# Optimization experiments

Measured on AMD Instinct MI355X. Metric: run time of the kernel, lower is better.

The kernel has to match this reference:

```python
import jax, jax.numpy as jnp
import numpy as np

NEG_BIG = -1.0e9


def setup_inputs() -> dict:
    key = jax.random.key(0)
    kq, kk, kv, km = jax.random.split(key, 4)
    B, Lq, Lk, D = 16, 2048, 2048, 128
    queries = jax.random.normal(kq, (B, Lq, D), dtype=jnp.float32)
    keys = jax.random.normal(kk, (B, Lk, D), dtype=jnp.float32)
    values = jax.random.normal(kv, (B, Lk, D), dtype=jnp.float32)
    mask = (jax.random.uniform(km, (Lk,)) > 0.8).astype(jnp.float32)
    return {"queries": queries, "keys": keys, "values": values, "mask": mask}


def reference(queries, keys, values, mask):
    d = keys.shape[-1]
    # scores: [B, Lq, Lk]
    scores = jnp.einsum("bqd,bkd->bqk", queries, keys) / jnp.sqrt(jnp.float32(d))
    masked = scores + mask[None, None, :] * NEG_BIG
    attn = jax.nn.softmax(masked, axis=-1)
    # dropout is identity in eval / p=0.0
    return jnp.einsum("bqk,bkd->bqd", attn, values)
```

## Files before the change

kernel.cpp:

```cpp
#include <hip/hip_runtime.h>
#include <hip/hip_bf16.h>


#define B_    16
#define LQ_   2048
#define LK_   2048
#define DIM_  128
#define NTH   256
#define SCALE_ 0.08838834764831845f
#define LOG2E_ 1.4426950408889634f
#define SC2_   (SCALE_ * LOG2E_)
#define NEGBIG -1.0e9f
#define PS 72

typedef __attribute__((ext_vector_type(8))) short bf16x8;
typedef __attribute__((ext_vector_type(4))) float f32x4;

#define GLDS(gsrc, ldst) \
  __builtin_amdgcn_global_load_lds( \
      (const __attribute__((address_space(1))) unsigned int*)(gsrc), \
      (__attribute__((address_space(3))) unsigned int*)(ldst), 16, 0, 0)

static __device__ __forceinline__ unsigned short f2bf(float f) {
    unsigned int u = __builtin_bit_cast(unsigned int, f);
    u += 0x7fff + ((u >> 16) & 1);
    return (unsigned short)(u >> 16);
}

__global__ __launch_bounds__(256) void build_idx(const float* __restrict__ Mk,
                                                 int* __restrict__ hdr,
                                                 int* __restrict__ idx)
{
    __shared__ int sc[256];
    int t = threadIdx.x;
    int keep[8], loc[8];
    int c = 0;
    #pragma unroll
    for (int j = 0; j < 8; ++j) {
        keep[j] = (Mk[t * 8 + j] < 0.5f) ? 1 : 0;
        loc[j] = c;
        c += keep[j];
    }
    sc[t] = c;
    __syncthreads();
    for (int off = 1; off < 256; off <<= 1) {
        int v = (t >= off) ? sc[t - off] : 0;
        __syncthreads();
        sc[t] += v;
        __syncthreads();
    }
    int base = sc[t] - c;
    #pragma unroll
    for (int j = 0; j < 8; ++j)
        if (keep[j]) idx[base + loc[j]] = t * 8 + j;
    if (t == 255) hdr[0] = sc[255];
}

__global__ __launch_bounds__(NTH) void pack_kv(
    const float* __restrict__ K, const float* __restrict__ V,
    const int* __restrict__ hdr, const int* __restrict__ idx,
    unsigned short* __restrict__ Kb, unsigned short* __restrict__ Vtb)
{
    const int cnt = hdr[0];
    int bid = blockIdx.x;
    if (bid < 2048) {
        int gid = bid * NTH + threadIdx.x;
        int c  = gid & 15;
        int r2 = (gid >> 4) & 63;
        int T  = gid >> 10;
        int slot = (r2 & 32) + 2 * (r2 & 15) + ((r2 >> 4) & 1);
        int j = (T & 31) * 64 + slot;
        int key = (j < cnt) ? idx[j] : 0;
        const float4* s4 = (const float4*)(K + ((size_t)(T >> 5) * LK_ + key) * DIM_ + c * 8);
        float4 a = s4[0], bq = s4[1];
        bf16x8 h = { (short)f2bf(a.x),  (short)f2bf(a.y),  (short)f2bf(a.z),  (short)f2bf(a.w),
                     (short)f2bf(bq.x), (short)f2bf(bq.y), (short)f2bf(bq.z), (short)f2bf(bq.w) };
        *(bf16x8*)(Kb + (size_t)T * 8192 + r2 * 128 + ((c ^ (r2 & 15)) * 8)) = h;
    } else {
        int T = bid - 2048;
        int w4 = threadIdx.x >> 6, lane = threadIdx.x & 63;
        const float* vb = V + (size_t)(T >> 5) * LK_ * DIM_;
        const int* ix = idx + (T & 31) * 64;
        int jbase = (T & 31) * 64;
        unsigned short* db = Vtb + (size_t)T * 8192;
        #pragma unroll
        for (int half = 0; half < 2; ++half) {
            int d = half * 64 + lane;
            #pragma unroll
            for (int cb = 0; cb < 8; cb += 4) {
                int c = cb + w4;
                float v[8];
                #pragma unroll
                for (int kk = 0; kk < 8; ++kk) {
                    int j = c * 8 + kk;
                    int key = (jbase + j < cnt) ? ix[j] : 0;
                    v[kk] = vb[(size_t)key * DIM_ + d];
                }
                bf16x8 h = { (short)f2bf(v[0]), (short)f2bf(v[1]), (short)f2bf(v[2]), (short)f2bf(v[3]),
                             (short)f2bf(v[4]), (short)f2bf(v[5]), (short)f2bf(v[6]), (short)f2bf(v[7]) };
                *(bf16x8*)(db + (c >> 2) * 4096 + d * 32 + (c & 3) * 8) = h;
            }
        }
    }
}

__global__ __launch_bounds__(NTH, 2) void attn_mfma6(
    const float* __restrict__ Q, const unsigned short* __restrict__ Kb,
    const unsigned short* __restrict__ Vtb, const int* __restrict__ hdr,
    float* __restrict__ O)
{
    __shared__ __align__(16) unsigned short sKa[8192];
    __shared__ __align__(16) unsigned short sKb_[8192];
    __shared__ __align__(16) unsigned short sP[64 * PS];
    __shared__ float sLp[64];

    const int tid  = threadIdx.x;
    const int w    = tid >> 6, lane = tid & 63;
    const int quad = lane >> 4, l15 = lane & 15;
    const int rg   = (w & 1) * 32;
    const int wh   = w >> 1;
    const int kh   = wh * 32;

    const int bid = blockIdx.x;
    const int grp = bid >> 3;
    const int b   = (bid & 7) + 8 * (grp & 1);
    const int q0  = (grp >> 1) * 64;

    const int cnt = hdr[0];
    const int nIter2 = (((cnt + 63) >> 6) + 1) & ~1;

    bf16x8 vone;
    #pragma unroll
    for (int j = 0; j < 8; ++j) vone[j] = (short)0x3F80;

    const int voff = wh * 4096 + l15 * 32 + quad * 8;

    bf16x8 aQ[2][4];
    {
        const float4* Qg = (const float4*)(Q + ((size_t)b * LQ_ + q0) * DIM_);
        #pragma unroll
        for (int h = 0; h < 2; ++h) {
            #pragma unroll
            for (int it = 0; it < 4; ++it) {
                int i2 = tid + it * NTH;
                int r = i2 >> 5, c4 = i2 & 31;
                float4 v = Qg[(h * 32 + r) * 32 + c4];
                ushort4 hh = { f2bf(v.x * SC2_), f2bf(v.y * SC2_),
                               f2bf(v.z * SC2_), f2bf(v.w * SC2_) };
                *(ushort4*)&sP[r * 128 + (((c4 >> 1) ^ (r & 15)) * 8) + (c4 & 1) * 4] = hh;
            }
            __syncthreads();
            if ((rg >> 5) == h) {
                #pragma unroll
                for (int rs = 0; rs < 2; ++rs)
                    #pragma unroll
                    for (int ks = 0; ks < 4; ++ks)
                        aQ[rs][ks] = *(const bf16x8*)&sP[(rs * 16 + l15) * 128 +
                                                         (((ks * 4 + quad) ^ l15) * 8)];
            }
            __syncthreads();
        }
    }

    {
        const char* ksrc = (const char*)Kb + (size_t)(b * 32) * 16384;
        #pragma unroll
        for (int j = 0; j < 4; ++j) {
            int o = (j * 4 + w) * 1024;
            GLDS(ksrc + o + lane * 16, (char*)sKa + o);
        }
    }
    __syncthreads();

    f32x4 acc[2][8], lacc[2];
    #pragma unroll
    for (int rs = 0; rs < 2; ++rs) {
        lacc[rs] = (f32x4){0.f, 0.f, 0.f, 0.f};
        #pragma unroll
        for (int dt = 0; dt < 8; ++dt) acc[rs][dt] = (f32x4){0.f, 0.f, 0.f, 0.f};
    }

#define TILE_BODY(CURK, NXTK, I) do {                                          \
         \
    const unsigned short* vsrc = Vtb + (size_t)(b * 32 + (I)) * 8192 + voff;   \
    bf16x8 bv[8];                                                              \
    _Pragma("unroll")                                                          \
    for (int dt = 0; dt < 8; ++dt) bv[dt] = *(const bf16x8*)(vsrc + dt * 512); \
    const int nxt = (I) + 1;                                                   \
    if (nxt < nIter2) {                                                        \
        const char* ksrc = (const char*)Kb + (size_t)(b * 32 + nxt) * 16384;   \
        _Pragma("unroll")                                                      \
        for (int j = 0; j < 4; ++j) {                                          \
            int o = (j * 4 + w) * 1024;                                        \
            GLDS(ksrc + o + lane * 16, (char*)(NXTK) + o);                     \
        }                                                                      \
    }                                                                          \
    f32x4 s_[2][2];                                                            \
    _Pragma("unroll")                                                          \
    for (int kt2 = 0; kt2 < 2; ++kt2) {                                        \
        f32x4 c0 = (f32x4){0.f,0.f,0.f,0.f}, c1 = (f32x4){0.f,0.f,0.f,0.f};   \
        _Pragma("unroll")                                                      \
        for (int ks = 0; ks < 4; ++ks) {                                       \
            bf16x8 bk = *(const bf16x8*)&(CURK)[(kh + kt2 * 16 + l15) * 128 +  \
                                                (((ks * 4 + quad) ^ l15) * 8)];\
            c0 = __builtin_amdgcn_mfma_f32_16x16x32_bf16(aQ[0][ks], bk, c0, 0,0,0); \
            c1 = __builtin_amdgcn_mfma_f32_16x16x32_bf16(aQ[1][ks], bk, c1, 0,0,0); \
        }                                                                      \
        int slot = (I) * 64 + kh + 2 * l15 + kt2;                              \
        bool kept = slot < cnt;                                                \
        _Pragma("unroll")                                                      \
        for (int r = 0; r < 4; ++r) {                                          \
            s_[0][kt2][r] = kept ? c0[r] : -1.0e30f;                           \
            s_[1][kt2][r] = kept ? c1[r] : -1.0e30f;                           \
        }                                                                      \
    }                                                                          \
    _Pragma("unroll")                                                          \
    for (int rs = 0; rs < 2; ++rs)                                             \
        _Pragma("unroll")                                                      \
        for (int r = 0; r < 4; ++r) {                                          \
            float p0 = __builtin_amdgcn_exp2f(s_[rs][0][r]);                   \
            float p1 = __builtin_amdgcn_exp2f(s_[rs][1][r]);                   \
            int row = rg + rs * 16 + quad * 4 + r;                             \
            unsigned pk = __builtin_amdgcn_perm(                               \
                __builtin_bit_cast(unsigned, p1),                              \
                __builtin_bit_cast(unsigned, p0), 0x07060302u);                \
            *(unsigned*)&sP[row * PS + kh + 2 * l15] = pk;                     \
        }                                                                      \
    {                                                                          \
        bf16x8 aP0 = *(const bf16x8*)&sP[(rg + l15) * PS + kh + quad * 8];     \
        bf16x8 aP1 = *(const bf16x8*)&sP[(rg + 16 + l15) * PS + kh + quad * 8];\
        lacc[0] = __builtin_amdgcn_mfma_f32_16x16x32_bf16(aP0, vone, lacc[0], 0,0,0); \
        lacc[1] = __builtin_amdgcn_mfma_f32_16x16x32_bf16(aP1, vone, lacc[1], 0,0,0); \
        _Pragma("unroll")                                                      \
        for (int dt = 0; dt < 8; ++dt) {                                       \
            acc[0][dt] = __builtin_amdgcn_mfma_f32_16x16x32_bf16(aP0, bv[dt], acc[0][dt], 0,0,0); \
            acc[1][dt] = __builtin_amdgcn_mfma_f32_16x16x32_bf16(aP1, bv[dt], acc[1][dt], 0,0,0); \
        }                                                                      \
    }                                                                          \
    __syncthreads();                                                           \
} while (0)

    for (int kk = 0; kk < nIter2; kk += 2) {
        TILE_BODY(sKa,  sKb_, kk);
        TILE_BODY(sKb_, sKa,  kk + 1);
    }
#undef TILE_BODY

    float* sOw = (rg == 0) ? (float*)sKa : (float*)sKb_;
    if (wh == 1) {
        #pragma unroll
        for (int rs = 0; rs < 2; ++rs)
            #pragma unroll
            for (int r = 0; r < 4; ++r) {
                int lrow = rs * 16 + quad * 4 + r;
                #pragma unroll
                for (int dt = 0; dt < 8; ++dt)
                    sOw[lrow * 128 + dt * 16 + l15] = acc[rs][dt][r];
                if (l15 == 0) sLp[rg + lrow] = lacc[rs][r];
            }
    }
    __syncthreads();
    if (wh == 0) {
        float* Og = O + ((size_t)b * LQ_ + q0 + rg) * DIM_;
        #pragma unroll
        for (int rs = 0; rs < 2; ++rs)
            #pragma unroll
            for (int r = 0; r < 4; ++r) {
                int lrow = rs * 16 + quad * 4 + r;
                float inv = 1.0f / (lacc[rs][r] + sLp[rg + lrow]);
                #pragma unroll
                for (int dt = 0; dt < 8; ++dt)
                    Og[(size_t)lrow * DIM_ + dt * 16 + l15] =
                        (acc[rs][dt][r] + sOw[lrow * 128 + dt * 16 + l15]) * inv;
            }
    }
}

#define QS 136
#define VS 72
__global__ __launch_bounds__(NTH, 2) void attn_fallback(
    const float* __restrict__ Q, const float* __restrict__ K,
    const float* __restrict__ V, const float* __restrict__ Mk,
    float* __restrict__ O)
{
    __shared__ __align__(16) unsigned short sQ[64][QS];
    __shared__ __align__(16) unsigned short sK[64][QS];
    __shared__ __align__(16) unsigned short sVt[DIM_][VS];
    __shared__ __align__(16) unsigned short sPf[64][VS];
    __shared__ float sB[64];

    const int tid  = threadIdx.x;
    const int w    = tid >> 6, lane = tid & 63;
    const int quad = lane >> 4, l15 = lane & 15;
    const int bid = blockIdx.x;
    const int grp = bid >> 3;
    const int b   = (bid & 7) + 8 * (grp & 1);
    const int q0  = (grp >> 1) * 64;

    {
        const float4* Qg = (const float4*)(Q + ((size_t)b * LQ_ + q0) * DIM_);
        #pragma unroll
        for (int it = 0; it < 8; ++it) {
            int i = tid + it * NTH;
            int r = i >> 5, c4 = i & 31;
            float4 v = Qg[r * 32 + c4];
            ushort4 h = { f2bf(v.x), f2bf(v.y), f2bf(v.z), f2bf(v.w) };
            *(ushort4*)&sQ[r][c4 * 4] = h;
        }
    }
    __syncthreads();
    bf16x8 aQ[4];
    #pragma unroll
    for (int ks = 0; ks < 4; ++ks)
        aQ[ks] = *(const bf16x8*)&sQ[w * 16 + l15][ks * 32 + quad * 8];

    float m_i[4], l_i[4];
    f32x4 acc[8];
    #pragma unroll
    for (int r = 0; r < 4; ++r) { m_i[r] = -3.0e38f; l_i[r] = 0.f; }
    #pragma unroll
    for (int dt = 0; dt < 8; ++dt) acc[dt] = (f32x4){0.f, 0.f, 0.f, 0.f};

    for (int k0 = 0; k0 < LK_; k0 += 64) {
        const float4* Kg = (const float4*)(K + ((size_t)b * LK_ + k0) * DIM_);
        const float4* Vg = (const float4*)(V + ((size_t)b * LK_ + k0) * DIM_);
        #pragma unroll
        for (int it = 0; it < 8; ++it) {
            int i = tid + it * NTH;
            int r = i >> 5, c4 = i & 31;
            float4 kv = Kg[r * 32 + c4];
            ushort4 h = { f2bf(kv.x), f2bf(kv.y), f2bf(kv.z), f2bf(kv.w) };
            *(ushort4*)&sK[r][c4 * 4] = h;
            float4 vv = Vg[r * 32 + c4];
            int d = c4 * 4;
            sVt[d + 0][r] = f2bf(vv.x);
            sVt[d + 1][r] = f2bf(vv.y);
            sVt[d + 2][r] = f2bf(vv.z);
            sVt[d + 3][r] = f2bf(vv.w);
        }
        if (tid < 64) sB[tid] = Mk[k0 + tid] * NEGBIG;
        __syncthreads();

        f32x4 s[4];
        #pragma unroll
        for (int kt = 0; kt < 4; ++kt) {
            f32x4 c = (f32x4){0.f, 0.f, 0.f, 0.f};
            #pragma unroll
            for (int ks = 0; ks < 4; ++ks) {
                bf16x8 bk = *(const bf16x8*)&sK[kt * 16 + l15][ks * 32 + quad * 8];
                c = __builtin_amdgcn_mfma_f32_16x16x32_bf16(aQ[ks], bk, c, 0, 0, 0);
            }
            float bias = sB[kt * 16 + l15];
            #pragma unroll
            for (int r = 0; r < 4; ++r) s[kt][r] = c[r] * SCALE_ + bias;
        }
        #pragma unroll
        for (int r = 0; r < 4; ++r) {
            float mx = fmaxf(fmaxf(s[0][r], s[1][r]), fmaxf(s[2][r], s[3][r]));
            #pragma unroll
            for (int off = 1; off < 16; off <<= 1) mx = fmaxf(mx, __shfl_xor(mx, off));
            float mn = fmaxf(m_i[r], mx);
            float al = __expf(m_i[r] - mn);
            m_i[r] = mn;
            float rsum = 0.f;
            #pragma unroll
            for (int kt = 0; kt < 4; ++kt) {
                float p = __expf(s[kt][r] - mn);
                rsum += p;
                sPf[w * 16 + quad * 4 + r][kt * 16 + l15] = f2bf(p);
            }
            #pragma unroll
            for (int off = 1; off < 16; off <<= 1) rsum += __shfl_xor(rsum, off);
            l_i[r] = l_i[r] * al + rsum;
            #pragma unroll
            for (int dt = 0; dt < 8; ++dt) acc[dt][r] *= al;
        }
        bf16x8 aP0 = *(const bf16x8*)&sPf[w * 16 + l15][quad * 8];
        bf16x8 aP1 = *(const bf16x8*)&sPf[w * 16 + l15][32 + quad * 8];
        #pragma unroll
        for (int dt = 0; dt < 8; ++dt) {
            bf16x8 bv0 = *(const bf16x8*)&sVt[dt * 16 + l15][quad * 8];
            bf16x8 bv1 = *(const bf16x8*)&sVt[dt * 16 + l15][32 + quad * 8];
            acc[dt] = __builtin_amdgcn_mfma_f32_16x16x32_bf16(aP0, bv0, acc[dt], 0, 0, 0);
            acc[dt] = __builtin_amdgcn_mfma_f32_16x16x32_bf16(aP1, bv1, acc[dt], 0, 0, 0);
        }
        __syncthreads();
    }
    float* Og = O + ((size_t)b * LQ_ + q0 + w * 16) * DIM_;
    #pragma unroll
    for (int r = 0; r < 4; ++r) {
        float inv = 1.0f / l_i[r];
        int row = quad * 4 + r;
        #pragma unroll
        for (int dt = 0; dt < 8; ++dt)
            Og[(size_t)row * DIM_ + dt * 16 + l15] = acc[dt][r] * inv;
    }
}

extern "C" void kernel_launch(void* const* d_in, const int* in_sizes, int n_in,
                              void* d_out, int out_size, void* d_ws, size_t ws_size,
                              hipStream_t stream)
{
    const float* Q  = (const float*)d_in[0];
    const float* K  = (const float*)d_in[1];
    const float* V  = (const float*)d_in[2];
    const float* Mk = (const float*)d_in[3];
    float* O = (float*)d_out;

    const size_t seg  = (size_t)B_ * LK_ * DIM_ * 2;
    const size_t need = 16384 + 2 * seg;
    if (ws_size >= need) {
        int* hdr = (int*)d_ws;
        int* idx = hdr + 16;
        unsigned short* Kb  = (unsigned short*)((char*)d_ws + 16384);
        unsigned short* Vtb = Kb + seg / 2;
        hipLaunchKernelGGL(build_idx, dim3(1),    dim3(256), 0, stream, Mk, hdr, idx);
        hipLaunchKernelGGL(pack_kv,   dim3(2560), dim3(NTH), 0, stream, K, V, hdr, idx, Kb, Vtb);
        hipLaunchKernelGGL(attn_mfma6, dim3(512), dim3(NTH), 0, stream, Q, Kb, Vtb, hdr, O);
    } else {
        hipLaunchKernelGGL(attn_fallback, dim3(512), dim3(NTH), 0, stream, Q, K, V, Mk, O);
    }
}
```

Baseline: 144.5 us.

## Fuse mask compaction into packing and stream K fragments directly to registers

Merges the single-block index build and the K/V packing kernel into one kernel. Each block recomputes the mask prefix scan in shared memory and transposes V through LDS. K is now stored in MFMA-fragment order, so the attention kernel loads K and V straight into double-buffered registers instead of staging K through LDS with global_load_lds. This removes one launch and the per-tile block barriers. The cost is more registers (risking occupancy at launch bounds 2) and redundant scans across 512 blocks.

New measurement: 155.4 us. 7.5% more time.

```diff
diff --git a/kernel.cpp b/kernel.cpp
--- a/kernel.cpp
+++ b/kernel.cpp
@@ -16,102 +16,96 @@
 typedef __attribute__((ext_vector_type(8))) short bf16x8;
 typedef __attribute__((ext_vector_type(4))) float f32x4;
 
-#define GLDS(gsrc, ldst) \
-  __builtin_amdgcn_global_load_lds( \
-      (const __attribute__((address_space(1))) unsigned int*)(gsrc), \
-      (__attribute__((address_space(3))) unsigned int*)(ldst), 16, 0, 0)
-
 static __device__ __forceinline__ unsigned short f2bf(float f) {
     unsigned int u = __builtin_bit_cast(unsigned int, f);
     u += 0x7fff + ((u >> 16) & 1);
     return (unsigned short)(u >> 16);
 }
 
-__global__ __launch_bounds__(256) void build_idx(const float* __restrict__ Mk,
-                                                 int* __restrict__ hdr,
-                                                 int* __restrict__ idx)
+__global__ __launch_bounds__(NTH) void pack_all(
+    const float* __restrict__ K, const float* __restrict__ V,
+    const float* __restrict__ Mk, int* __restrict__ hdr,
+    unsigned short* __restrict__ Kb, unsigned short* __restrict__ Vtb)
 {
+    __shared__ int sIdx[2048];
     __shared__ int sc[256];
-    int t = threadIdx.x;
+    __shared__ unsigned short sV[64 * 136];
+
+    const int tid = threadIdx.x;
+    const int T = blockIdx.x;
+    const int b = T >> 5, t = T & 31;
+
     int keep[8], loc[8];
     int c = 0;
     #pragma unroll
     for (int j = 0; j < 8; ++j) {
-        keep[j] = (Mk[t * 8 + j] < 0.5f) ? 1 : 0;
+        keep[j] = (Mk[tid * 8 + j] < 0.5f) ? 1 : 0;
         loc[j] = c;
         c += keep[j];
     }
-    sc[t] = c;
+    sc[tid] = c;
     __syncthreads();
     for (int off = 1; off < 256; off <<= 1) {
-        int v = (t >= off) ? sc[t - off] : 0;
+        int v = (tid >= off) ? sc[tid - off] : 0;
         __syncthreads();
-        sc[t] += v;
+        sc[tid] += v;
         __syncthreads();
     }
-    int base = sc[t] - c;
+    const int base = sc[tid] - c;
     #pragma unroll
     for (int j = 0; j < 8; ++j)
-        if (keep[j]) idx[base + loc[j]] = t * 8 + j;
-    if (t == 255) hdr[0] = sc[255];
+        if (keep[j]) sIdx[base + loc[j]] = tid * 8 + j;
+    __syncthreads();
+    const int cnt = sc[255];
+    if (T == 0 && tid == 0) hdr[0] = cnt;
+
+    const float* Kbase = K + (size_t)b * LK_ * DIM_;
+    unsigned short* kdst = Kb + (size_t)T * 8192;
+    #pragma unroll
+    for (int it = 0; it < 8; ++it) {
+        int i = tid + it * NTH;
+        int sp = i >> 5, c4 = i & 31;
+        int wh = sp >> 5, kt2 = (sp >> 4) & 1, l15 = sp & 15;
+        int g = t * 64 + wh * 32 + 2 * l15 + kt2;
+        int key = (g < cnt) ? sIdx[g] : 0;
+        float4 v = *(const float4*)(Kbase + (size_t)key * DIM_ + c4 * 4);
+        ushort4 h = { f2bf(v.x), f2bf(v.y), f2bf(v.z), f2bf(v.w) };
+        int ks = c4 >> 3, quad = (c4 >> 1) & 3;
+        *(ushort4*)(kdst + wh * 4096 + kt2 * 2048 + ks * 512 +
+                    quad * 128 + l15 * 8 + (c4 & 1) * 4) = h;
+    }
+
+    const float* Vbase = V + (size_t)b * LK_ * DIM_;
+    #pragma unroll
+    for (int it = 0; it < 8; ++it) {
+        int i = tid + it * NTH;
+        int slot = i >> 5, c4 = i & 31;
+        int g = t * 64 + slot;
+        int key = (g < cnt) ? sIdx[g] : 0;
+        float4 v = *(const float4*)(Vbase + (size_t)key * DIM_ + c4 * 4);
+        ushort4 h = { f2bf(v.x), f2bf(v.y), f2bf(v.z), f2bf(v.w) };
+        *(ushort4*)&sV[slot * 136 + c4 * 4] = h;
+    }
+    __syncthreads();
+    unsigned short* vdst = Vtb + (size_t)T * 8192;
+    const int d = tid & 127, wh2 = tid >> 7;
+    #pragma unroll
+    for (int quad = 0; quad < 4; ++quad) {
+        bf16x8 h;
+        #pragma unroll
+        for (int j = 0; j < 8; ++j)
+            h[j] = (short)sV[(wh2 * 32 + quad * 8 + j) * 136 + d];
+        *(bf16x8*)(vdst + wh2 * 4096 + d * 32 + quad * 8) = h;
+    }
 }
 
-__global__ __launch_bounds__(NTH) void pack_kv(
-    const float* __restrict__ K, const float* __restrict__ V,
-    const int* __restrict__ hdr, const int* __restrict__ idx,
-    unsigned short* __restrict__ Kb, unsigned short* __restrict__ Vtb)
-{
-    const int cnt = hdr[0];
-    int bid = blockIdx.x;
-    if (bid < 2048) {
-        int gid = bid * NTH + threadIdx.x;
-        int c  = gid & 15;
-        int r2 = (gid >> 4) & 63;
-        int T  = gid >> 10;
-        int slot = (r2 & 32) + 2 * (r2 & 15) + ((r2 >> 4) & 1);
-        int j = (T & 31) * 64 + slot;
-        int key = (j < cnt) ? idx[j] : 0;
-        const float4* s4 = (const float4*)(K + ((size_t)(T >> 5) * LK_ + key) * DIM_ + c * 8);
-        float4 a = s4[0], bq = s4[1];
-        bf16x8 h = { (short)f2bf(a.x),  (short)f2bf(a.y),  (short)f2bf(a.z),  (short)f2bf(a.w),
-                     (short)f2bf(bq.x), (short)f2bf(bq.y), (short)f2bf(bq.z), (short)f2bf(bq.w) };
-        *(bf16x8*)(Kb + (size_t)T * 8192 + r2 * 128 + ((c ^ (r2 & 15)) * 8)) = h;
-    } else {
-        int T = bid - 2048;
-        int w4 = threadIdx.x >> 6, lane = threadIdx.x & 63;
-        const float* vb = V + (size_t)(T >> 5) * LK_ * DIM_;
-        const int* ix = idx + (T & 31) * 64;
-        int jbase = (T & 31) * 64;
-        unsigned short* db = Vtb + (size_t)T * 8192;
-        #pragma unroll
-        for (int half = 0; half < 2; ++half) {
-            int d = half * 64 + lane;
-            #pragma unroll
-            for (int cb = 0; cb < 8; cb += 4) {
-                int c = cb + w4;
-                float v[8];
-                #pragma unroll
-                for (int kk = 0; kk < 8; ++kk) {
-                    int j = c * 8 + kk;
-                    int key = (jbase + j < cnt) ? ix[j] : 0;
-                    v[kk] = vb[(size_t)key * DIM_ + d];
-                }
-                bf16x8 h = { (short)f2bf(v[0]), (short)f2bf(v[1]), (short)f2bf(v[2]), (short)f2bf(v[3]),
-                             (short)f2bf(v[4]), (short)f2bf(v[5]), (short)f2bf(v[6]), (short)f2bf(v[7]) };
-                *(bf16x8*)(db + (c >> 2) * 4096 + d * 32 + (c & 3) * 8) = h;
-            }
-        }
-    }
-}
-
-__global__ __launch_bounds__(NTH, 2) void attn_mfma6(
+__global__ __launch_bounds__(NTH, 2) void attn_mfma7(
     const float* __restrict__ Q, const unsigned short* __restrict__ Kb,
     const unsigned short* __restrict__ Vtb, const int* __restrict__ hdr,
     float* __restrict__ O)
 {
-    __shared__ __align__(16) unsigned short sKa[8192];
-    __shared__ __align__(16) unsigned short sKb_[8192];
     __shared__ __align__(16) unsigned short sP[64 * PS];
+    __shared__ float sO[64 * 128];
     __shared__ float sLp[64];
 
     const int tid  = threadIdx.x;
@@ -134,6 +128,7 @@
     for (int j = 0; j < 8; ++j) vone[j] = (short)0x3F80;
 
     const int voff = wh * 4096 + l15 * 32 + quad * 8;
+    const int koff = wh * 4096 + lane * 8;
 
     bf16x8 aQ[2][4];
     {
@@ -162,16 +157,6 @@
         }
     }
 
-    {
-        const char* ksrc = (const char*)Kb + (size_t)(b * 32) * 16384;
-        #pragma unroll
-        for (int j = 0; j < 4; ++j) {
-            int o = (j * 4 + w) * 1024;
-            GLDS(ksrc + o + lane * 16, (char*)sKa + o);
-        }
-    }
-    __syncthreads();
-
     f32x4 acc[2][8], lacc[2];
     #pragma unroll
     for (int rs = 0; rs < 2; ++rs) {
@@ -180,31 +165,30 @@
         for (int dt = 0; dt < 8; ++dt) acc[rs][dt] = (f32x4){0.f, 0.f, 0.f, 0.f};
     }
 
-#define TILE_BODY(CURK, NXTK, I) do {                                          \
-         \
-    const unsigned short* vsrc = Vtb + (size_t)(b * 32 + (I)) * 8192 + voff;   \
-    bf16x8 bv[8];                                                              \
+#define LOADKV(DK, DV, I) do {                                                 \
+    const unsigned short* kbp = Kb + (size_t)(b * 32 + (I)) * 8192 + koff;     \
     _Pragma("unroll")                                                          \
-    for (int dt = 0; dt < 8; ++dt) bv[dt] = *(const bf16x8*)(vsrc + dt * 512); \
+    for (int kt2 = 0; kt2 < 2; ++kt2)                                          \
+        _Pragma("unroll")                                                      \
+        for (int ks = 0; ks < 4; ++ks)                                         \
+            DK[kt2][ks] = *(const bf16x8*)(kbp + kt2 * 2048 + ks * 512);       \
+    const unsigned short* vbp = Vtb + (size_t)(b * 32 + (I)) * 8192 + voff;    \
+    _Pragma("unroll")                                                          \
+    for (int dt = 0; dt < 8; ++dt)                                             \
+        DV[dt] = *(const bf16x8*)(vbp + dt * 512);                             \
+} while (0)
+
+#define TILE_BODY(CK, CV, NK, NV, I) do {                                      \
     const int nxt = (I) + 1;                                                   \
-    if (nxt < nIter2) {                                                        \
-        const char* ksrc = (const char*)Kb + (size_t)(b * 32 + nxt) * 16384;   \
-        _Pragma("unroll")                                                      \
-        for (int j = 0; j < 4; ++j) {                                          \
-            int o = (j * 4 + w) * 1024;                                        \
-            GLDS(ksrc + o + lane * 16, (char*)(NXTK) + o);                     \
-        }                                                                      \
-    }                                                                          \
+    if (nxt < nIter2) LOADKV(NK, NV, nxt);                                     \
     f32x4 s_[2][2];                                                            \
     _Pragma("unroll")                                                          \
     for (int kt2 = 0; kt2 < 2; ++kt2) {                                        \
         f32x4 c0 = (f32x4){0.f,0.f,0.f,0.f}, c1 = (f32x4){0.f,0.f,0.f,0.f};   \
         _Pragma("unroll")                                                      \
         for (int ks = 0; ks < 4; ++ks) {                                       \
-            bf16x8 bk = *(const bf16x8*)&(CURK)[(kh + kt2 * 16 + l15) * 128 +  \
-                                                (((ks * 4 + quad) ^ l15) * 8)];\
-            c0 = __builtin_amdgcn_mfma_f32_16x16x32_bf16(aQ[0][ks], bk, c0, 0,0,0); \
-            c1 = __builtin_amdgcn_mfma_f32_16x16x32_bf16(aQ[1][ks], bk, c1, 0,0,0); \
+            c0 = __builtin_amdgcn_mfma_f32_16x16x32_bf16(aQ[0][ks], CK[kt2][ks], c0, 0,0,0); \
+            c1 = __builtin_amdgcn_mfma_f32_16x16x32_bf16(aQ[1][ks], CK[kt2][ks], c1, 0,0,0); \
         }                                                                      \
         int slot = (I) * 64 + kh + 2 * l15 + kt2;                              \
         bool kept = slot < cnt;                                                \
@@ -233,30 +217,31 @@
         lacc[1] = __builtin_amdgcn_mfma_f32_16x16x32_bf16(aP1, vone, lacc[1], 0,0,0); \
         _Pragma("unroll")                                                      \
         for (int dt = 0; dt < 8; ++dt) {                                       \
-            acc[0][dt] = __builtin_amdgcn_mfma_f32_16x16x32_bf16(aP0, bv[dt], acc[0][dt], 0,0,0); \
-            acc[1][dt] = __builtin_amdgcn_mfma_f32_16x16x32_bf16(aP1, bv[dt], acc[1][dt], 0,0,0); \
+            acc[0][dt] = __builtin_amdgcn_mfma_f32_16x16x32_bf16(aP0, CV[dt], acc[0][dt], 0,0,0); \
+            acc[1][dt] = __builtin_amdgcn_mfma_f32_16x16x32_bf16(aP1, CV[dt], acc[1][dt], 0,0,0); \
         }                                                                      \
     }                                                                          \
-    __syncthreads();                                                           \
 } while (0)
 
+    bf16x8 bkA[2][4], bvA[8], bkB[2][4], bvB[8];
+    LOADKV(bkA, bvA, 0);
     for (int kk = 0; kk < nIter2; kk += 2) {
-        TILE_BODY(sKa,  sKb_, kk);
-        TILE_BODY(sKb_, sKa,  kk + 1);
+        TILE_BODY(bkA, bvA, bkB, bvB, kk);
+        TILE_BODY(bkB, bvB, bkA, bvA, kk + 1);
     }
 #undef TILE_BODY
-
-    float* sOw = (rg == 0) ? (float*)sKa : (float*)sKb_;
+#undef LOADKV
+
     if (wh == 1) {
         #pragma unroll
         for (int rs = 0; rs < 2; ++rs)
             #pragma unroll
             for (int r = 0; r < 4; ++r) {
-                int lrow = rs * 16 + quad * 4 + r;
+                int lrow = rg + rs * 16 + quad * 4 + r;
                 #pragma unroll
                 for (int dt = 0; dt < 8; ++dt)
-                    sOw[lrow * 128 + dt * 16 + l15] = acc[rs][dt][r];
-                if (l15 == 0) sLp[rg + lrow] = lacc[rs][r];
+                    sO[lrow * 128 + dt * 16 + l15] = acc[rs][dt][r];
+                if (l15 == 0) sLp[lrow] = lacc[rs][r];
             }
     }
     __syncthreads();
@@ -271,7 +256,7 @@
                 #pragma unroll
                 for (int dt = 0; dt < 8; ++dt)
                     Og[(size_t)lrow * DIM_ + dt * 16 + l15] =
-                        (acc[rs][dt][r] + sOw[lrow * 128 + dt * 16 + l15]) * inv;
+                        (acc[rs][dt][r] + sO[(rg + lrow) * 128 + dt * 16 + l15]) * inv;
             }
     }
 }
@@ -411,12 +396,10 @@
     const size_t need = 16384 + 2 * seg;
     if (ws_size >= need) {
         int* hdr = (int*)d_ws;
-        int* idx = hdr + 16;
         unsigned short* Kb  = (unsigned short*)((char*)d_ws + 16384);
         unsigned short* Vtb = Kb + seg / 2;
-        hipLaunchKernelGGL(build_idx, dim3(1),    dim3(256), 0, stream, Mk, hdr, idx);
-        hipLaunchKernelGGL(pack_kv,   dim3(2560), dim3(NTH), 0, stream, K, V, hdr, idx, Kb, Vtb);
-        hipLaunchKernelGGL(attn_mfma6, dim3(512), dim3(NTH), 0, stream, Q, Kb, Vtb, hdr, O);
+        hipLaunchKernelGGL(pack_all,   dim3(512), dim3(NTH), 0, stream, K, V, Mk, hdr, Kb, Vtb);
+        hipLaunchKernelGGL(attn_mfma7, dim3(512), dim3(NTH), 0, stream, Q, Kb, Vtb, hdr, O);
     } else {
         hipLaunchKernelGGL(attn_fallback, dim3(512), dim3(NTH), 0, stream, Q, K, V, Mk, O);
     }
```
